# Performance work log

Hardware: AMD Instinct MI355X
Metric: run time of the kernel (lower is better)

The kernel has to match this reference:

```python
import jax, jax.numpy as jnp
import numpy as np

V, D, N, K, T, S = 128000, 128, 4, 4, 16, 5
EPS = 1e-10


def setup_inputs() -> dict:
    key = jax.random.key(0)
    k = jax.random.split(key, 5)
    return {
        "E": jax.random.normal(k[0], (V, D), jnp.float32) * 0.02,
        "bases": jax.random.normal(k[1], (K, N, D, D), jnp.float32) * (1.5 / np.sqrt(D)),
        "tension": jax.random.normal(k[2], (K, N, N), jnp.float32) * 0.1,
        "temperature": jnp.ones((K,), jnp.float32),
        "target_sim": jnp.full((K,), -1.0 / (N - 1), jnp.float32),
        "step_size": jnp.full((K,), 0.1, jnp.float32),
        "gate_logit": jnp.full((K,), -2.0, jnp.float32),
        "decay_base": jnp.asarray(0.8, jnp.float32),
        "sensitivity": jnp.asarray(1.0, jnp.float32),
        "noise": jax.random.normal(k[3], (T, K, S, N, D), jnp.float32),
        "tokens": jax.random.randint(k[4], (T,), 0, V),
    }


def reference(E, bases, tension, temperature, target_sim, step_size, gate_logit,
              decay_base, sensitivity, noise, tokens):
    mask = 1.0 - jnp.eye(N, dtype=E.dtype)
    temp = jnp.clip(jnp.abs(temperature), 0.01, None)
    # gauge interaction weights per foam: softmax over bubbles, self-interaction masked
    interaction = jax.nn.softmax(-tension / temp[:, None, None], axis=-1) * mask  # [K,N,N]
    step = jnp.clip(jnp.abs(step_size), 0.001, 0.5)           # [K]
    gate = jax.nn.sigmoid(gate_logit)                          # [K] noise gate
    sens = jnp.abs(sensitivity)

    def equilibrate(state0, B, inter, tgt, stp, g, nz):
        # state0 [N,D]; B [N,D,D] per-bubble bases; nz [S,N,D] pre-drawn perturbations
        def body(state, eps):
            expr = jnp.einsum('nd,nkd->nk', state, B)          # state_i @ basis_i.T
            expr_n = expr / (jnp.linalg.norm(expr, axis=-1, keepdims=True) + EPS)
            cos = expr_n @ expr_n.T                            # [N,N] pairwise cos-sim
            fmag = (cos - tgt) * inter                         # [N,N] force magnitudes
            diff = expr[:, None, :] - expr[None, :, :]         # [N,N,D]
            diff_n = diff / (jnp.linalg.norm(diff, axis=-1, keepdims=True) + EPS)
            f_shared = (fmag[..., None] * diff_n).sum(axis=1)  # [N,D]
            f_local = jnp.einsum('nk,nkd->nd', f_shared, B)    # back to local gauge
            scale = jnp.linalg.norm(state, axis=-1).mean() + EPS
            return state + stp * f_local + g * eps * scale * 0.01, None
        state, _ = jax.lax.scan(body, state0, nz)
        return state

    def foam_step(x, memory, B, inter, tgt, stp, g, nz):
        # x [D]; memory [N,D]
        mem_mean = memory.mean(axis=0)
        mem_norm = jnp.linalg.norm(mem_mean) + EPS
        x_norm = jnp.linalg.norm(x) + EPS
        nov = 1.0 - (x * mem_mean).sum() / (x_norm * mem_norm)
        novelty = jnp.where(mem_norm > 1e-8, nov, 1.0)
        decay = jax.nn.sigmoid(decay_base - sens * novelty)
        xm = x + decay * mem_mean
        eq = equilibrate(jnp.broadcast_to(xm, (N, D)), B, inter, tgt, stp, g, nz)
        rho = (eq.T @ eq) / ((eq * eq).sum() + EPS)            # trace-normalized density
        mem_new = decay * memory + (1.0 - decay) * eq
        return rho, mem_new

    xs_tok = E[tokens]                                         # [T,D]

    def token_step(memories, inp):
        x, nz_t = inp
        rhos, memories = jax.vmap(foam_step, in_axes=(None, 0, 0, 0, 0, 0, 0, 0))(
            x, memories, bases, interaction, target_sim, step, gate, nz_t)
        rho_mix = rhos.mean(axis=0)                            # [D,D]
        eig = jnp.clip(jnp.linalg.eigvalsh(rho_mix), 1e-12, None)
        eig = eig / eig.sum()
        logits = ((E @ rho_mix) * E).sum(axis=-1)              # born rule [V]
        logp = jax.nn.log_softmax(logits)
        probs = jnp.exp(logp)
        S_rho = -(eig * jnp.clip(jnp.log(eig), -100.0, None)).sum()
        H_tok = -(probs * jnp.clip(logp, -100.0, None)).sum()
        return memories, (probs, S_rho, H_tok, H_tok - S_rho)

    mem0 = jnp.zeros((K, N, D), E.dtype)
    _, (probs, S_rho, H_tok, F_tok) = jax.lax.scan(token_step, mem0, (xs_tok, noise))
    return probs, S_rho, H_tok, F_tok
```

## Files before the change

### kernel.cpp

```cpp
#include <hip/hip_runtime.h>
#include <math.h>

#define V_ 128000
#define D_ 128
#define N_ 4
#define K_ 4
#define T_ 16
#define S_ 5
#define EPSF 1e-10f

#define WS_G      0
#define WS_BEPS   262144
#define WS_BX     917504
#define WS_EQBALL 954368
#define WS_INTER  977408
#define WS_WK     977472
#define WS_SRHO   977728
#define WS_LNZ    977744
#define WS_ZPART  977760
#define WS_HPART  1009760

typedef __attribute__((ext_vector_type(8))) short short8v;
typedef __attribute__((ext_vector_type(4))) float float4v;

__device__ __forceinline__ short bfb(float x) {
    unsigned u = __float_as_uint(x);
    u += 0x7fffu + ((u >> 16) & 1u);
    return (short)(u >> 16);
}

__device__ __forceinline__ void jpair(int x, int r, int& ox, bool& isp) {
    if (x == 15) { ox = r % 15; isp = true; return; }
    int s = x - r; s %= 15; if (s < 0) s += 15;
    if (s == 0) { ox = 15; isp = false; return; }
    int o = 2 * r - x; o %= 15; if (o < 0) o += 15;
    ox = o;
    isp = (s <= 7);
}

__device__ __forceinline__ void rotfast(float app, float aqq, float apq, float& c, float& s) {
    c = 1.f; s = 0.f;
    if (fabsf(apq) > 1e-20f) {
        float tau = (aqq - app) * 0.5f * __builtin_amdgcn_rcpf(apq);
        float sq1 = __builtin_amdgcn_sqrtf(1.f + tau * tau);
        float den = tau + ((tau >= 0.f) ? sq1 : -sq1);
        float tt = __builtin_amdgcn_rcpf(den);
        c = __builtin_amdgcn_rsqf(1.f + tt * tt);
        s = tt * c;
    }
}

__global__ __launch_bounds__(256)
void i2_prep(const float* __restrict__ bases, const float* __restrict__ E,
             const float* __restrict__ noise, const int* __restrict__ tokens,
             const float* __restrict__ tension, const float* __restrict__ temperature,
             float* __restrict__ ws)
{
    int tid = threadIdx.x;
    if (blockIdx.x == 64) {
        if (tid < 4) {
            int k = tid;
            float temp = fmaxf(fabsf(temperature[k]), 0.01f);
            for (int i = 0; i < 4; ++i) {
                float v[4]; float mx = -1e30f;
                for (int j = 0; j < 4; ++j) { v[j] = -tension[k*16 + i*4 + j] / temp; mx = fmaxf(mx, v[j]); }
                float se = 0.f;
                for (int j = 0; j < 4; ++j) { v[j] = expf(v[j] - mx); se += v[j]; }
                for (int j = 0; j < 4; ++j) ws[WS_INTER + k*16 + i*4 + j] = (i == j) ? 0.0f : v[j] / se;
            }
        }
        return;
    }
    int kn = blockIdx.x >> 2, q = blockIdx.x & 3;
    int k = kn >> 2, n = kn & 3;
    __shared__ __align__(16) float Blds[128 * 132];
    const float4* B4 = (const float4*)(bases + (size_t)kn * 16384);
    for (int idx = tid; idx < 4096; idx += 256) {
        int jrow = idx >> 5, c = idx & 31;
        float4 v = B4[jrow * 32 + c];
        *((float4*)&Blds[jrow * 132 + c * 4]) = v;
    }
    __syncthreads();
    int j1 = q * 32 + (tid >> 3);
    int l = tid & 7;
    float accg[16];
#pragma unroll
    for (int i = 0; i < 16; ++i) accg[i] = 0.f;
    for (int c = 0; c < 32; ++c) {
        float4 b1 = *((const float4*)&Blds[j1 * 132 + c * 4]);
#pragma unroll
        for (int i = 0; i < 16; ++i) {
            float4 b2 = *((const float4*)&Blds[(l + 8 * i) * 132 + c * 4]);
            accg[i] += b1.x * b2.x + b1.y * b2.y + b1.z * b2.z + b1.w * b2.w;
        }
    }
#pragma unroll
    for (int i = 0; i < 16; ++i) {
        int j2 = l + 8 * i;
        ws[WS_G + (((size_t)kn * 32 + (j2 >> 2)) * 128 + j1) * 4 + (j2 & 3)] = accg[i];
    }
    __shared__ __align__(16) float vecl[128];
    __shared__ float vred[2][128];
    int jv = tid & 127, ch = tid >> 7;
    for (int vi = q * 24; vi < q * 24 + 24; ++vi) {
        const float* src; int dstoff;
        if (vi < 16) {
            int tt = vi;
            src = E + (size_t)tokens[tt] * 128;
            dstoff = WS_BX + (tt * 4 + k) * 512 + n * 128;
        } else {
            int r2 = vi - 16; int tt = r2 / 5, s2 = r2 % 5;
            size_t off = (size_t)(((tt * 4 + k) * 5 + s2) * 4 + n) * 128;
            src = noise + off;
            dstoff = WS_BEPS + (int)off;
        }
        if (tid < 32) ((float4*)vecl)[tid] = ((const float4*)src)[tid];
        __syncthreads();
        float a2 = 0.f;
        for (int c = ch * 16; c < ch * 16 + 16; ++c) {
            float4 bv = *((const float4*)&Blds[jv * 132 + c * 4]);
            float4 xv = ((const float4*)vecl)[c];
            a2 += bv.x * xv.x + bv.y * xv.y + bv.z * xv.z + bv.w * xv.w;
        }
        vred[ch][jv] = a2;
        __syncthreads();
        if (tid < 128) ws[dstoff + tid] = vred[0][tid] + vred[1][tid];
        __syncthreads();
    }
}

__global__ __launch_bounds__(512, 2)
void kap_all(const float* __restrict__ E, const float* __restrict__ noise,
             const int* __restrict__ tokens, const float* __restrict__ bases,
             const float* __restrict__ target_sim, const float* __restrict__ step_size,
             const float* __restrict__ gate_logit, const float* __restrict__ decay_base,
             const float* __restrict__ sensitivity, float* __restrict__ ws)
{
    const int k = blockIdx.x;
    const int tid = threadIdx.x;
    const int w = tid >> 6;
    const int n = w & 3;
    const int h = w >> 2;
    const int lane = tid & 63;
    const int d0 = lane, d1 = lane + 64;
    const int dG = h * 64 + lane;
    const int kn = k * 4 + n;

    __shared__ float xl[128];
    __shared__ float mlL[128];
    __shared__ __align__(16) float aL[4][128];
    __shared__ float exL[4][128];
    __shared__ float bmmL[4][128];
    __shared__ float interL[16];
    __shared__ float diagP[4], sP[4];
    __shared__ float sq7[4][2];

    float4 gg[32];
    const float4* G4 = (const float4*)(ws + WS_G);
#pragma unroll
    for (int c = 0; c < 32; ++c) gg[c] = G4[((size_t)kn * 32 + c) * 128 + dG];

    if (tid < 16) interL[tid] = ws[WS_INTER + k * 16 + tid];
    if (tid < 128) mlL[tid] = 0.f;
    bmmL[n][dG] = 0.f;

    const float tgt = target_sim[k];
    const float stp = fminf(fmaxf(fabsf(step_size[k]), 0.001f), 0.5f);
    const float gate = 1.0f / (1.0f + expf(-gate_logit[k]));
    const float dbase = decay_base[0];
    const float sens = fabsf(sensitivity[0]);

    float xr = (tid < 128) ? E[(size_t)tokens[0] * 128 + tid] : 0.f;
    __syncthreads();
    float w_inter[4];
#pragma unroll
    for (int m = 0; m < 4; ++m) w_inter[m] = interL[n * 4 + m];

#pragma unroll 1
    for (int t = 0; t < T_; ++t) {
        if (tid < 128) xl[tid] = xr;
        __syncthreads();
        if (t + 1 < T_ && tid < 128) xr = E[(size_t)tokens[t + 1] * 128 + tid];

        float bep0[5], bep1[5], no0[5], no1[5];
#pragma unroll
        for (int s = 0; s < 5; ++s) {
            int nz = (((t * 4 + k) * 5 + s) * 4 + n) * 128;
            bep0[s] = ws[WS_BEPS + nz + d0]; bep1[s] = ws[WS_BEPS + nz + d1];
            no0[s] = noise[nz + d0];         no1[s] = noise[nz + d1];
        }
        float bx0 = ws[WS_BX + (t * 4 + k) * 512 + n * 128 + d0];
        float bx1 = ws[WS_BX + (t * 4 + k) * 512 + n * 128 + d1];

        float x0 = xl[d0], x1 = xl[d1], m0 = mlL[d0], m1 = mlL[d1];
        float vx = x0 * x0 + x1 * x1, vm = m0 * m0 + m1 * m1, vd = x0 * m0 + x1 * m1;
        for (int m = 32; m; m >>= 1) { vx += __shfl_xor(vx, m); vm += __shfl_xor(vm, m); vd += __shfl_xor(vd, m); }
        float xnorm = sqrtf(vx) + EPSF, mnorm = sqrtf(vm) + EPSF;
        float nov = 1.0f - vd / (xnorm * mnorm);
        float novelty = (mnorm > 1e-8f) ? nov : 1.0f;
        const float dec = 1.0f / (1.0f + expf(-(dbase - sens * novelty)));

        float bm0 = bmmL[n][d0], bm1 = bmmL[n][d1];
        float e00 = bx0 + dec * bm0, e01 = bx1 + dec * bm1;
        float u0 = x0 + dec * m0, u1 = x1 + dec * m1;
        float a0 = 0.f, a1 = 0.f, be0 = 0.f, be1 = 0.f;
        exL[n][dG] = (h == 0) ? e00 : e01;
        __syncthreads();

        for (int s = 0; s < 5; ++s) {
            float em0[4], em1[4];
#pragma unroll
            for (int m = 0; m < 4; ++m) { em0[m] = exL[m][d0]; em1[m] = exL[m][d1]; }
            float ex0 = em0[n], ex1 = em1[n];
            float r[5];
#pragma unroll
            for (int m = 0; m < 4; ++m) r[m] = ex0 * em0[m] + ex1 * em1[m];
            float t4 = u0 * u0 + u1 * u1;
            float t5 = (e00 + be0) * a0 + (e01 + be1) * a1;
            float t6 = a0 * (ex0 - e00 - be0) + a1 * (ex1 - e01 - be1);
            r[4] = t4 + 2.f * t5 + t6;
#pragma unroll
            for (int m2 = 32; m2; m2 >>= 1) {
#pragma unroll
                for (int q = 0; q < 5; ++q) r[q] += __shfl_xor(r[q], m2);
            }
            float sn = sqrtf(fmaxf(r[4], 0.f));
            if (lane == 0 && h == 0) { diagP[n] = r[n]; sP[n] = sn; }
            __syncthreads();
            float ssum = ((sP[0] + sP[1]) + sP[2]) + sP[3];
            float cn = gate * (0.25f * ssum + EPSF) * 0.01f;

            float Pnn = r[n];
            float enn = sqrtf(fmaxf(Pnn, 0.f)) + EPSF;
            float fsh0 = 0.f, fsh1 = 0.f;
#pragma unroll
            for (int m = 0; m < 4; ++m) {
                float Pmm = diagP[m];
                float Pnm = r[m];
                float enm = sqrtf(fmaxf(Pmm, 0.f)) + EPSF;
                float cosnm = Pnm / (enn * enm);
                float fm = (cosnm - tgt) * w_inter[m];
                float dnn = sqrtf(fmaxf(Pnn - 2.f * Pnm + Pmm, 0.f)) + EPSF;
                float wq = fm / dnn;
                fsh0 += wq * (ex0 - em0[m]);
                fsh1 += wq * (ex1 - em1[m]);
            }
            a0 += stp * fsh0; a1 += stp * fsh1;
            be0 += cn * bep0[s]; be1 += cn * bep1[s];
            u0 += cn * no0[s];   u1 += cn * no1[s];
            aL[n][d0] = a0; aL[n][d1] = a1;
            const float4* a4 = (const float4*)aL[n];
            float y = 0.f;
#pragma unroll
            for (int c = 0; c < 32; ++c) {
                float4 av = a4[c];
                y += gg[c].x * av.x + gg[c].y * av.y + gg[c].z * av.z + gg[c].w * av.w;
            }
            float exn = ((h == 0) ? e00 : e01) + y + ((h == 0) ? be0 : be1);
            exL[n][dG] = exn;
            __syncthreads();
        }

        {
            const float* Bp = bases + (size_t)kn * 16384;
            float acc = 0.f;
#pragma unroll 8
            for (int j = 0; j < 128; ++j) acc += aL[n][j] * Bp[(size_t)j * 128 + dG];
            float eq = ((h == 0) ? u0 : u1) + acc;
            ws[WS_BEPS + t * 10240 + k * 2560 + n * 128 + dG] = eq;
            unsigned short* eqb = (unsigned short*)(ws + WS_EQBALL);
            {
                int c2 = dG >> 5, lg = (dG >> 3) & 3, j8 = dG & 7;
                eqb[t * 2048 + (c2 * 64 + lg * 16 + kn) * 8 + j8] = (unsigned short)bfb(eq);
            }
            float sq = eq * eq;
            for (int m = 32; m; m >>= 1) sq += __shfl_xor(sq, m);
            if (lane == 0) sq7[n][h] = sq;
            exL[n][dG] = eq;
            __syncthreads();
            if (tid < 4) {
                float s4 = (sq7[0][0] + sq7[0][1]) + (sq7[1][0] + sq7[1][1])
                         + (sq7[2][0] + sq7[2][1]) + (sq7[3][0] + sq7[3][1]);
                ws[WS_WK + t * 16 + 4 * k + tid] = 1.0f / (4.0f * (s4 + EPSF));
            }
            if (n == 0) {
                float eqm = 0.25f * (exL[0][dG] + exL[1][dG] + exL[2][dG] + exL[3][dG]);
                mlL[dG] = dec * mlL[dG] + (1.f - dec) * eqm;
            }
            __syncthreads();
            const float4* Br = (const float4*)(bases + (size_t)kn * 16384 + (size_t)dG * 128);
            const float4* mm4 = (const float4*)mlL;
            float bacc = 0.f;
#pragma unroll 8
            for (int c = 0; c < 32; ++c) {
                float4 mv = mm4[c];
                float4 bv = Br[c];
                bacc += bv.x * mv.x + bv.y * mv.y + bv.z * mv.z + bv.w * mv.w;
            }
            bmmL[n][dG] = bacc;
        }
    }
}

__global__ __launch_bounds__(256, 2)
void mega(const float* __restrict__ E, float* __restrict__ ws, float* __restrict__ out)
{
    int b = blockIdx.x, tid = threadIdx.x;
    __shared__ __align__(16) short8v eqL[2048];
    if (b < 16) {
        int tt = b;
        __shared__ float Gsh[256];
        __shared__ float Am[16 * 20];
        __shared__ float cR[16], sR[16];
        {
            int i = tid >> 4, j = tid & 15;
            const float4* ra = (const float4*)(ws + WS_BEPS + tt * 10240 + (i >> 2) * 2560 + (i & 3) * 128);
            const float4* rb = (const float4*)(ws + WS_BEPS + tt * 10240 + (j >> 2) * 2560 + (j & 3) * 128);
            float dp = 0.f;
#pragma unroll 8
            for (int c = 0; c < 32; ++c) {
                float4 a = ra[c], b2 = rb[c];
                dp += a.x * b2.x + a.y * b2.y + a.z * b2.z + a.w * b2.w;
            }
            Gsh[tid] = dp;
        }
        __syncthreads();
        if (tid >= 64) return;
        const float* G = Gsh;
        int i0 = tid >> 2, j40 = (tid & 3) * 4;
        float wv4[4];
#pragma unroll
        for (int kk = 0; kk < 4; ++kk) {
            float ss = G[(4*kk+0)*17] + G[(4*kk+1)*17] + G[(4*kk+2)*17] + G[(4*kk+3)*17];
            wv4[kk] = 1.0f / (4.0f * (ss + EPSF));
        }
#pragma unroll
        for (int m = 0; m < 4; ++m) {
            int jjv = j40 + m;
            Am[i0 * 20 + jjv] = sqrtf(wv4[i0 >> 2] * wv4[jjv >> 2]) * G[i0 * 16 + jjv];
        }
        for (int sw = 0; sw < 6; ++sw) {
            for (int r = 0; r < 15; ++r) {
                if (tid < 8) {
                    int p, q;
                    if (tid == 0) { p = 15; q = r % 15; }
                    else { p = (r + tid) % 15; q = (r - tid + 15) % 15; }
                    float c, s;
                    rotfast(Am[p * 20 + p], Am[q * 20 + q], Am[p * 20 + q], c, s);
                    cR[p] = c; sR[p] = -s;
                    cR[q] = c; sR[q] = s;
                }
                int oi; bool ip; jpair(i0, r, oi, ip);
                float ci = cR[i0], siS = sR[i0];
                float nv[4];
#pragma unroll
                for (int m = 0; m < 4; ++m) {
                    int jjv = j40 + m;
                    int oj; bool jp2; jpair(jjv, r, oj, jp2);
                    float cj = cR[jjv], sjS = sR[jjv];
                    float a00 = Am[i0 * 20 + jjv], a01 = Am[i0 * 20 + oj];
                    float a10 = Am[oi * 20 + jjv], a11 = Am[oi * 20 + oj];
                    nv[m] = ci*cj*a00 + ci*sjS*a01 + siS*cj*a10 + siS*sjS*a11;
                }
#pragma unroll
                for (int m = 0; m < 4; ++m) Am[i0 * 20 + j40 + m] = nv[m];
            }
        }
        if (tid == 0) {
            float tot = 112.0f * 1e-12f;
            float lc[16];
            for (int a2 = 0; a2 < 16; ++a2) { lc[a2] = fmaxf(Am[a2 * 20 + a2], 1e-12f); tot += lc[a2]; }
            float S = 0.f;
            for (int a2 = 0; a2 < 16; ++a2) { float pp = lc[a2] / tot; S -= pp * fmaxf(logf(pp), -100.f); }
            float p0 = 1e-12f / tot;
            S -= 112.f * p0 * fmaxf(logf(p0), -100.f);
            out[(size_t)T_ * V_ + tt] = S;
            ws[WS_SRHO + tt] = S;
        }
        return;
    }
    int b2 = b - 16;
    int pass = b2 / 500;
    int bb = b2 - pass * 500;
    int tok0 = pass * 8;
    int lane = tid & 63, wv = tid >> 6;
    {
        const float4* src = (const float4*)(ws + WS_EQBALL) + tok0 * 256;
        float4* dst = (float4*)eqL;
#pragma unroll
        for (int i = 0; i < 8; ++i) dst[tid + i * 256] = src[tid + i * 256];
    }
    float wk[8], zl[8];
#pragma unroll
    for (int tk = 0; tk < 8; ++tk) {
        wk[tk] = ws[WS_WK + (tok0 + tk) * 16 + (lane & 15)];
        zl[tk] = 0.f;
    }
    __syncthreads();
    int tilebase = (bb * 4 + wv) * 64;
#pragma unroll
    for (int it = 0; it < 4; ++it) {
        int rowB = tilebase + it * 16;
        const float* Erow = E + (size_t)(rowB + (lane & 15)) * 128 + ((lane >> 4) * 8);
        float4v acc[8];
#pragma unroll
        for (int tk = 0; tk < 8; ++tk) acc[tk] = (float4v){0.f, 0.f, 0.f, 0.f};
#pragma unroll
        for (int c2 = 0; c2 < 4; ++c2) {
            float4 e0 = *((const float4*)(Erow + c2 * 32));
            float4 e1 = *((const float4*)(Erow + c2 * 32 + 4));
            short8v a;
            a[0] = bfb(e0.x); a[1] = bfb(e0.y); a[2] = bfb(e0.z); a[3] = bfb(e0.w);
            a[4] = bfb(e1.x); a[5] = bfb(e1.y); a[6] = bfb(e1.z); a[7] = bfb(e1.w);
#pragma unroll
            for (int tk = 0; tk < 8; ++tk)
                acc[tk] = __builtin_amdgcn_mfma_f32_16x16x32_bf16(a, eqL[tk * 256 + c2 * 64 + lane], acc[tk], 0, 0, 0);
        }
#pragma unroll
        for (int tk = 0; tk < 8; ++tk) {
            float l0 = wk[tk] * acc[tk][0] * acc[tk][0];
            float l1 = wk[tk] * acc[tk][1] * acc[tk][1];
            float l2 = wk[tk] * acc[tk][2] * acc[tk][2];
            float l3 = wk[tk] * acc[tk][3] * acc[tk][3];
#pragma unroll
            for (int m = 1; m <= 8; m <<= 1) {
                l0 += __shfl_xor(l0, m); l1 += __shfl_xor(l1, m);
                l2 += __shfl_xor(l2, m); l3 += __shfl_xor(l3, m);
            }
            if ((lane & 15) == 0) {
                float4 st; st.x = l0; st.y = l1; st.z = l2; st.w = l3;
                *((float4*)(out + (size_t)(tok0 + tk) * V_ + rowB + (lane >> 4) * 4)) = st;
                zl[tk] += __expf(l0) + __expf(l1) + __expf(l2) + __expf(l3);
            }
        }
    }
#pragma unroll
    for (int tk = 0; tk < 8; ++tk) {
        float z = zl[tk];
        z += __shfl_xor(z, 16); z += __shfl_xor(z, 32);
        if (lane == 0) ws[WS_ZPART + (tok0 + tk) * 2000 + bb * 4 + wv] = z;
    }
}

__global__ __launch_bounds__(256)
void zk(float* __restrict__ ws)
{
    int b = blockIdx.x, tid = threadIdx.x;
    double s = 0.0;
    for (int i = tid; i < 2000; i += 256) s += (double)ws[WS_ZPART + b * 2000 + i];
    for (int m = 32; m; m >>= 1) s += __shfl_xor(s, m);
    __shared__ double sr[4];
    if ((tid & 63) == 0) sr[tid >> 6] = s;
    __syncthreads();
    if (tid == 0) ws[WS_LNZ + b] = (float)log(sr[0] + sr[1] + sr[2] + sr[3]);
}

__global__ __launch_bounds__(256)
void fin1(float* __restrict__ ws, float* __restrict__ out)
{
    int b = blockIdx.x, tid = threadIdx.x;
    int tt = b / 125, blk = b - tt * 125;
    int v = blk * 1024 + tid * 4;
    float lnZ = ws[WS_LNZ + tt];
    float* po = out + (size_t)tt * V_ + v;
    float4 l4 = *((const float4*)po);
    float lp0 = l4.x - lnZ, lp1 = l4.y - lnZ, lp2 = l4.z - lnZ, lp3 = l4.w - lnZ;
    float p0 = __expf(lp0), p1 = __expf(lp1), p2 = __expf(lp2), p3 = __expf(lp3);
    float4 st; st.x = p0; st.y = p1; st.z = p2; st.w = p3;
    *((float4*)po) = st;
    float hp = p0 * fmaxf(lp0, -100.f) + p1 * fmaxf(lp1, -100.f)
             + p2 * fmaxf(lp2, -100.f) + p3 * fmaxf(lp3, -100.f);
    for (int m = 32; m; m >>= 1) hp += __shfl_xor(hp, m);
    __shared__ float hr[4];
    if ((tid & 63) == 0) hr[tid >> 6] = hp;
    __syncthreads();
    if (tid == 0) ws[WS_HPART + tt * 125 + blk] = hr[0] + hr[1] + hr[2] + hr[3];
}

__global__ __launch_bounds__(128)
void f2_final(float* __restrict__ ws, float* __restrict__ out)
{
    int t = blockIdx.x, tid = threadIdx.x;
    float s = (tid < 125) ? ws[WS_HPART + t * 125 + tid] : 0.f;
    for (int m = 32; m; m >>= 1) s += __shfl_xor(s, m);
    __shared__ float sr[2];
    if ((tid & 63) == 0) sr[tid >> 6] = s;
    __syncthreads();
    if (tid == 0) {
        float H = -(sr[0] + sr[1]);
        float S = ws[WS_SRHO + t];
        out[(size_t)T_ * V_ + T_ + t] = H;
        out[(size_t)T_ * V_ + 2 * T_ + t] = H - S;
    }
}

extern "C" void kernel_launch(void* const* d_in, const int* in_sizes, int n_in,
                              void* d_out, int out_size, void* d_ws, size_t ws_size,
                              hipStream_t stream)
{
    (void)in_sizes; (void)n_in; (void)out_size; (void)ws_size;
    const float* E           = (const float*)d_in[0];
    const float* bases       = (const float*)d_in[1];
    const float* tension     = (const float*)d_in[2];
    const float* temperature = (const float*)d_in[3];
    const float* target_sim  = (const float*)d_in[4];
    const float* step_size   = (const float*)d_in[5];
    const float* gate_logit  = (const float*)d_in[6];
    const float* decay_base  = (const float*)d_in[7];
    const float* sensitivity = (const float*)d_in[8];
    const float* noise       = (const float*)d_in[9];
    const int*   tokens      = (const int*)d_in[10];
    float* out = (float*)d_out;
    float* ws  = (float*)d_ws;

    i2_prep<<<65, 256, 0, stream>>>(bases, E, noise, tokens, tension, temperature, ws);
    kap_all<<<4, 512, 0, stream>>>(E, noise, tokens, bases, target_sim, step_size,
                                   gate_logit, decay_base, sensitivity, ws);
    mega<<<1016, 256, 0, stream>>>(E, ws, out);
    zk<<<16, 256, 0, stream>>>(ws);
    fin1<<<T_ * 125, 256, 0, stream>>>(ws, out);
    f2_final<<<T_, 128, 0, stream>>>(ws, out);
}
```

Measured before the change: 600.0 us.

## Split kap_all matvecs across two thread halves with 1024-thread blocks

Doubles the kap_all block from 512 to 1024 threads and splits each 128-long reduction (the G matvec in the inner step, the basis back-projection and the memory projection) into two halves, one per thread group. The partial sums are combined through shared memory. This is meant to shorten the serial latency of the sequential recurrence, which runs on only 4 blocks, and to cut per-thread register use by halving the gg array. In exchange it adds an extra __syncthreads per inner step and per token, plus some duplicated work across the groups.

```diff
diff --git a/kernel.cpp b/kernel.cpp
--- a/kernel.cpp
+++ b/kernel.cpp
@@ -129,7 +129,7 @@
     }
 }
 
-__global__ __launch_bounds__(512, 2)
+__global__ __launch_bounds__(1024, 1)
 void kap_all(const float* __restrict__ E, const float* __restrict__ noise,
              const int* __restrict__ tokens, const float* __restrict__ bases,
              const float* __restrict__ target_sim, const float* __restrict__ step_size,
@@ -140,7 +140,8 @@
     const int tid = threadIdx.x;
     const int w = tid >> 6;
     const int n = w & 3;
-    const int h = w >> 2;
+    const int h = (w >> 2) & 1;
+    const int p = w >> 3;
     const int lane = tid & 63;
     const int d0 = lane, d1 = lane + 64;
     const int dG = h * 64 + lane;
@@ -150,19 +151,20 @@
     __shared__ float mlL[128];
     __shared__ __align__(16) float aL[4][128];
     __shared__ float exL[4][128];
-    __shared__ float bmmL[4][128];
+    __shared__ float ypL[2][4][128];
+    __shared__ float bpart[2][4][128];
     __shared__ float interL[16];
     __shared__ float diagP[4], sP[4];
     __shared__ float sq7[4][2];
 
-    float4 gg[32];
+    float4 gg[16];
     const float4* G4 = (const float4*)(ws + WS_G);
 #pragma unroll
-    for (int c = 0; c < 32; ++c) gg[c] = G4[((size_t)kn * 32 + c) * 128 + dG];
+    for (int c = 0; c < 16; ++c) gg[c] = G4[((size_t)kn * 32 + 16 * p + c) * 128 + dG];
 
     if (tid < 16) interL[tid] = ws[WS_INTER + k * 16 + tid];
     if (tid < 128) mlL[tid] = 0.f;
-    bmmL[n][dG] = 0.f;
+    bpart[p][n][dG] = 0.f;
 
     const float tgt = target_sim[k];
     const float stp = fminf(fmaxf(fabsf(step_size[k]), 0.001f), 0.5f);
@@ -200,7 +202,8 @@
         float novelty = (mnorm > 1e-8f) ? nov : 1.0f;
         const float dec = 1.0f / (1.0f + expf(-(dbase - sens * novelty)));
 
-        float bm0 = bmmL[n][d0], bm1 = bmmL[n][d1];
+        float bm0 = bpart[0][n][d0] + bpart[1][n][d0];
+        float bm1 = bpart[0][n][d1] + bpart[1][n][d1];
         float e00 = bx0 + dec * bm0, e01 = bx1 + dec * bm1;
         float u0 = x0 + dec * m0, u1 = x1 + dec * m1;
         float a0 = 0.f, a1 = 0.f, be0 = 0.f, be1 = 0.f;
@@ -225,7 +228,7 @@
                 for (int q = 0; q < 5; ++q) r[q] += __shfl_xor(r[q], m2);
             }
             float sn = sqrtf(fmaxf(r[4], 0.f));
-            if (lane == 0 && h == 0) { diagP[n] = r[n]; sP[n] = sn; }
+            if (lane == 0 && h == 0 && p == 0) { diagP[n] = r[n]; sP[n] = sn; }
             __syncthreads();
             float ssum = ((sP[0] + sP[1]) + sP[2]) + sP[3];
             float cn = gate * (0.25f * ssum + EPSF) * 0.01f;
@@ -252,11 +255,14 @@
             const float4* a4 = (const float4*)aL[n];
             float y = 0.f;
 #pragma unroll
-            for (int c = 0; c < 32; ++c) {
-                float4 av = a4[c];
+            for (int c = 0; c < 16; ++c) {
+                float4 av = a4[16 * p + c];
                 y += gg[c].x * av.x + gg[c].y * av.y + gg[c].z * av.z + gg[c].w * av.w;
             }
-            float exn = ((h == 0) ? e00 : e01) + y + ((h == 0) ? be0 : be1);
+            ypL[p][n][dG] = y;
+            __syncthreads();
+            float yfull = ypL[0][n][dG] + ypL[1][n][dG];
+            float exn = ((h == 0) ? e00 : e01) + yfull + ((h == 0) ? be0 : be1);
             exL[n][dG] = exn;
             __syncthreads();
         }
@@ -265,17 +271,19 @@
             const float* Bp = bases + (size_t)kn * 16384;
             float acc = 0.f;
 #pragma unroll 8
-            for (int j = 0; j < 128; ++j) acc += aL[n][j] * Bp[(size_t)j * 128 + dG];
-            float eq = ((h == 0) ? u0 : u1) + acc;
-            ws[WS_BEPS + t * 10240 + k * 2560 + n * 128 + dG] = eq;
-            unsigned short* eqb = (unsigned short*)(ws + WS_EQBALL);
-            {
+            for (int j = 64 * p; j < 64 * p + 64; ++j) acc += aL[n][j] * Bp[(size_t)j * 128 + dG];
+            ypL[p][n][dG] = acc;
+            __syncthreads();
+            float eq = ((h == 0) ? u0 : u1) + (ypL[0][n][dG] + ypL[1][n][dG]);
+            if (p == 0) {
+                ws[WS_BEPS + t * 10240 + k * 2560 + n * 128 + dG] = eq;
+                unsigned short* eqb = (unsigned short*)(ws + WS_EQBALL);
                 int c2 = dG >> 5, lg = (dG >> 3) & 3, j8 = dG & 7;
                 eqb[t * 2048 + (c2 * 64 + lg * 16 + kn) * 8 + j8] = (unsigned short)bfb(eq);
             }
             float sq = eq * eq;
             for (int m = 32; m; m >>= 1) sq += __shfl_xor(sq, m);
-            if (lane == 0) sq7[n][h] = sq;
+            if (lane == 0 && p == 0) sq7[n][h] = sq;
             exL[n][dG] = eq;
             __syncthreads();
             if (tid < 4) {
@@ -283,7 +291,7 @@
                          + (sq7[2][0] + sq7[2][1]) + (sq7[3][0] + sq7[3][1]);
                 ws[WS_WK + t * 16 + 4 * k + tid] = 1.0f / (4.0f * (s4 + EPSF));
             }
-            if (n == 0) {
+            if (n == 0 && p == 0) {
                 float eqm = 0.25f * (exL[0][dG] + exL[1][dG] + exL[2][dG] + exL[3][dG]);
                 mlL[dG] = dec * mlL[dG] + (1.f - dec) * eqm;
             }
@@ -292,12 +300,12 @@
             const float4* mm4 = (const float4*)mlL;
             float bacc = 0.f;
 #pragma unroll 8
-            for (int c = 0; c < 32; ++c) {
+            for (int c = 16 * p; c < 16 * p + 16; ++c) {
                 float4 mv = mm4[c];
                 float4 bv = Br[c];
                 bacc += bv.x * mv.x + bv.y * mv.y + bv.z * mv.z + bv.w * mv.w;
             }
-            bmmL[n][dG] = bacc;
+            bpart[p][n][dG] = bacc;
         }
     }
 }
@@ -514,8 +522,8 @@
     float* ws  = (float*)d_ws;
 
     i2_prep<<<65, 256, 0, stream>>>(bases, E, noise, tokens, tension, temperature, ws);
-    kap_all<<<4, 512, 0, stream>>>(E, noise, tokens, bases, target_sim, step_size,
-                                   gate_logit, decay_base, sensitivity, ws);
+    kap_all<<<4, 1024, 0, stream>>>(E, noise, tokens, bases, target_sim, step_size,
+                                    gate_logit, decay_base, sensitivity, ws);
     mega<<<1016, 256, 0, stream>>>(E, ws, out);
     zk<<<16, 256, 0, stream>>>(ws);
     fin1<<<T_ * 125, 256, 0, stream>>>(ws, out);
```

New measurement: 892.0 us. +48.7%, slower.
